# Optimization experiments

Hardware: AMD Instinct MI355X
Metric: run time of the kernel (lower is better)

## Reference

```python
import jax, jax.numpy as jnp
import numpy as np

THRESHOLD = 0.5
NEG_POS_RATIO = 3


def cxcy_to_xy(c):
    return jnp.concatenate([c[..., :2] - c[..., 2:] / 2.0, c[..., :2] + c[..., 2:] / 2.0], axis=-1)


def xy_to_cxcy(b):
    return jnp.concatenate([(b[..., :2] + b[..., 2:]) / 2.0, b[..., 2:] - b[..., :2]], axis=-1)


def cxcy_to_gcxgcy(c, p):
    # standard SSD encoding with variances (0.1, 0.2)
    return jnp.concatenate([
        (c[..., :2] - p[..., :2]) / (p[..., 2:] / 10.0),
        jnp.log(c[..., 2:] / p[..., 2:]) * 5.0,
    ], axis=-1)


def jaccard(a, b):
    # a: [n,4] xy boxes, b: [m,4] xy boxes -> [n,m] IoU
    lo = jnp.maximum(a[:, None, :2], b[None, :, :2])
    hi = jnp.minimum(a[:, None, 2:], b[None, :, 2:])
    wh = jnp.clip(hi - lo, 0.0)
    inter = wh[..., 0] * wh[..., 1]
    area_a = (a[:, 2] - a[:, 0]) * (a[:, 3] - a[:, 1])
    area_b = (b[:, 2] - b[:, 0]) * (b[:, 3] - b[:, 1])
    return inter / (area_a[:, None] + area_b[None, :] - inter)


def match_one(boxes_i, labels_i, priors_xy, priors_cxcy):
    # boxes_i: [O,4], labels_i: [O] -> true_locs [P,4], true_classes [P]
    n_obj = boxes_i.shape[0]
    ov = jaccard(boxes_i, priors_xy)                 # [O, P]
    ov_per_prior = ov.max(axis=0)                    # [P]
    obj_idx = jnp.argmax(ov, axis=0)                 # [P]
    prior_per_obj = jnp.argmax(ov, axis=1)           # [O]
    # force each object to own its best prior (scatter overwrite)
    obj_idx = obj_idx.at[prior_per_obj].set(jnp.arange(n_obj))
    ov_per_prior = ov_per_prior.at[prior_per_obj].set(1.0)
    lab = labels_i[obj_idx]                          # [P]
    lab = jnp.where(ov_per_prior < THRESHOLD, 0, lab)
    true_locs = cxcy_to_gcxgcy(xy_to_cxcy(boxes_i[obj_idx]), priors_cxcy)
    return true_locs, lab


def setup_inputs() -> dict:
    key = jax.random.key(0)
    ks = jax.random.split(key, 7)
    B, P, C, O = 64, 8732, 81, 32
    predicted_locs = jax.random.normal(ks[0], (B, P, 4), jnp.float32)
    predicted_scores = jax.random.normal(ks[1], (B, P, C), jnp.float32)
    ctr = jax.random.uniform(ks[2], (B, O, 2), jnp.float32, 0.2, 0.8)
    wh = jax.random.uniform(ks[3], (B, O, 2), jnp.float32, 0.05, 0.3)
    boxes = jnp.concatenate([ctr - wh / 2.0, ctr + wh / 2.0], axis=-1)  # valid xy boxes
    labels = jax.random.randint(ks[4], (B, O), 1, C)                    # nonzero object classes
    pctr = jax.random.uniform(ks[5], (P, 2), jnp.float32, 0.05, 0.95)
    pwh = jax.random.uniform(ks[6], (P, 2), jnp.float32, 0.05, 0.5)
    priors_cxcy = jnp.concatenate([pctr, pwh], axis=-1)
    return {
        'predicted_locs': predicted_locs,
        'predicted_scores': predicted_scores,
        'boxes': boxes,
        'labels': labels,
        'priors_cxcy': priors_cxcy,
    }


def reference(predicted_locs, predicted_scores, boxes, labels, priors_cxcy):
    priors_xy = cxcy_to_xy(priors_cxcy)
    true_locs, true_classes = jax.vmap(match_one, in_axes=(0, 0, None, None))(
        boxes, labels, priors_xy, priors_cxcy)       # [B,P,4], [B,P]

    log_probs = jax.nn.log_softmax(predicted_scores, axis=2)   # [B,P,C]
    bg_loss = -log_probs[:, :, 0]                               # mining score (detached in torch)

    pos_mask = true_classes > 0                                 # [B,P]
    num_pos = pos_mask.sum(axis=1, keepdims=True)               # [B,1]
    num_neg = NEG_POS_RATIO * num_pos
    mined = jnp.where(pos_mask, -jnp.inf, bg_loss)
    idx = jnp.argsort(-mined, axis=1)
    order = jnp.argsort(idx, axis=1)                            # rank of each prior by hardness
    neg_mask = order < num_neg
    mask = pos_mask | neg_mask

    # cross-entropy (sum over selected priors)
    ce = -jnp.take_along_axis(log_probs, true_classes[..., None], axis=2)[..., 0]  # [B,P]
    classification_loss = jnp.sum(ce * mask)

    # smooth-L1 (beta=1, sum over positive priors)
    diff = jnp.abs(predicted_locs - true_locs)
    sl1 = jnp.where(diff < 1.0, 0.5 * diff * diff, diff - 0.5)  # [B,P,4]
    smooth_l1_loss = jnp.sum(sl1.sum(axis=-1) * pos_mask)

    n = num_pos.sum().astype(predicted_locs.dtype)
    return classification_loss / n, smooth_l1_loss / n
```

## Files before the change

kernel.cpp:

```cpp
#include <hip/hip_runtime.h>
#include <stdint.h>

#define NB 64
#define NP 8732
#define NO 32
#define NC 81
#define NTOT (NB*NP)
#define THRESH 0.5f

typedef unsigned long long ull;

__global__ void k_init(float* cls_acc, float* sl1_acc, int* n_acc) {
    if (threadIdx.x == 0) { *cls_acc = 0.f; *sl1_acc = 0.f; *n_acc = 0; }
}

__global__ __launch_bounds__(512)
void k_match(const float4* __restrict__ boxes4, const int* __restrict__ labels,
             const float4* __restrict__ priors4, const float4* __restrict__ plocs4,
             int* __restrict__ lab_ws, int* __restrict__ numpos_ws,
             float* __restrict__ sl1_acc, int* __restrict__ n_acc)
{
#pragma clang fp contract(off)
    const int b   = blockIdx.x;
    const int tid = threadIdx.x;
    const int lane = tid & 63, wv = tid >> 6;

    __shared__ float         ov_s[NP];
    __shared__ unsigned char oi_s[NP];
    __shared__ float bx[NO][4];
    __shared__ float barea[NO];
    __shared__ int   blab[NO];
    __shared__ int   ppo[NO];
    __shared__ ull   red[8][8];
    __shared__ float redf[8];
    __shared__ int   redi[8];

    if (tid < NO) {
        float4 bb = boxes4[b*NO + tid];
        bx[tid][0] = bb.x; bx[tid][1] = bb.y; bx[tid][2] = bb.z; bx[tid][3] = bb.w;
        barea[tid] = (bb.z - bb.x) * (bb.w - bb.y);
        blab[tid]  = labels[b*NO + tid];
    }
    __syncthreads();

    for (int c = 0; c < 4; ++c) {
        ull bkey[8];
#pragma unroll
        for (int o8 = 0; o8 < 8; ++o8) bkey[o8] = 0ull;

        for (int p = tid; p < NP; p += 512) {
            float4 pr = priors4[p];
            float px1 = pr.x - pr.z*0.5f, py1 = pr.y - pr.w*0.5f;
            float px2 = pr.x + pr.z*0.5f, py2 = pr.y + pr.w*0.5f;
            float parea = (px2-px1)*(py2-py1);
            float bestv; int besto;
            if (c == 0) { bestv = -1.0f; besto = 0; }
            else        { bestv = ov_s[p]; besto = oi_s[p]; }
#pragma unroll
            for (int o8 = 0; o8 < 8; ++o8) {
                const int o = c*8 + o8;
                float lx = fmaxf(bx[o][0], px1), ly = fmaxf(bx[o][1], py1);
                float hx = fminf(bx[o][2], px2), hy = fminf(bx[o][3], py2);
                float w = fmaxf(hx - lx, 0.0f), h = fmaxf(hy - ly, 0.0f);
                float inter = w*h;
                float iou = inter / ((barea[o] + parea) - inter);
                if (iou > bestv) { bestv = iou; besto = o; }
                ull key = ((ull)__float_as_uint(iou) << 32) | (unsigned int)(~p);
                if (key > bkey[o8]) bkey[o8] = key;
            }
            ov_s[p] = bestv;
            oi_s[p] = (unsigned char)besto;
        }
#pragma unroll
        for (int o8 = 0; o8 < 8; ++o8) {
            ull k = bkey[o8];
            for (int off = 32; off > 0; off >>= 1) {
                ull other = __shfl_down(k, (unsigned)off);
                if (other > k) k = other;
            }
            if (lane == 0) red[o8][wv] = k;
        }
        __syncthreads();
        if (tid < 8) {
            ull k = red[tid][0];
#pragma unroll
            for (int w = 1; w < 8; ++w) if (red[tid][w] > k) k = red[tid][w];
            ppo[c*8 + tid] = (int)(~(unsigned int)(k & 0xFFFFFFFFull));
        }
        __syncthreads();
    }

    if (tid == 0) {
        for (int o = 0; o < NO; ++o) {
            int p = ppo[o];
            oi_s[p] = (unsigned char)o;
            ov_s[p] = 1.0f;
        }
    }
    __syncthreads();

    int cnt = 0; float sl1 = 0.0f;
    for (int p = tid; p < NP; p += 512) {
        float ov = ov_s[p];
        int   oi = oi_s[p];
        int   lb = (ov < THRESH) ? 0 : blab[oi];
        lab_ws[b*NP + p] = lb;
        if (lb > 0) {
            cnt++;
            float x1 = bx[oi][0], y1 = bx[oi][1], x2 = bx[oi][2], y2 = bx[oi][3];
            float bcx = (x1+x2)*0.5f, bcy = (y1+y2)*0.5f;
            float bw = x2-x1, bh = y2-y1;
            float4 pr = priors4[p];
            float g0 = (bcx - pr.x) / (pr.z / 10.0f);
            float g1 = (bcy - pr.y) / (pr.w / 10.0f);
            float g2 = logf(bw / pr.z) * 5.0f;
            float g3 = logf(bh / pr.w) * 5.0f;
            float4 pl = plocs4[(size_t)b*NP + p];
            float d0 = fabsf(pl.x-g0), d1 = fabsf(pl.y-g1);
            float d2 = fabsf(pl.z-g2), d3 = fabsf(pl.w-g3);
            sl1 += (d0 < 1.f ? 0.5f*d0*d0 : d0-0.5f);
            sl1 += (d1 < 1.f ? 0.5f*d1*d1 : d1-0.5f);
            sl1 += (d2 < 1.f ? 0.5f*d2*d2 : d2-0.5f);
            sl1 += (d3 < 1.f ? 0.5f*d3*d3 : d3-0.5f);
        }
    }
    for (int off = 32; off > 0; off >>= 1) {
        cnt += __shfl_down(cnt, (unsigned)off);
        sl1 += __shfl_down(sl1, (unsigned)off);
    }
    if (lane == 0) { redi[wv] = cnt; redf[wv] = sl1; }
    __syncthreads();
    if (tid == 0) {
        int c = 0; float s = 0.f;
#pragma unroll
        for (int w = 0; w < 8; ++w) { c += redi[w]; s += redf[w]; }
        numpos_ws[b] = c;
        atomicAdd(n_acc, c);
        atomicAdd(sl1_acc, s);
    }
}

#define CLS_BLOCKS 2048
__global__ __launch_bounds__(256)
void k_cls(const float* __restrict__ scores, const int* __restrict__ lab_ws,
           unsigned int* __restrict__ mined, float* __restrict__ cls_acc)
{
    const int lane = threadIdx.x & 63, wv = threadIdx.x >> 6;
    const int wave_gid = blockIdx.x*4 + wv;
    const int nw = CLS_BLOCKS*4;
    float ce_acc = 0.f;

    for (int r = wave_gid; r < NTOT; r += nw) {
        const float* s = scores + (size_t)r*NC;
        float v0 = s[lane];
        float v1 = (lane < NC-64) ? s[64+lane] : -INFINITY;
        float m = fmaxf(v0, v1);
#pragma unroll
        for (int off = 32; off > 0; off >>= 1) m = fmaxf(m, __shfl_xor(m, off));
        float e = expf(v0 - m) + ((lane < NC-64) ? expf(v1 - m) : 0.f);
#pragma unroll
        for (int off = 32; off > 0; off >>= 1) e += __shfl_xor(e, off);
        float lse = m + logf(e);

        int lb = lab_ws[r];
        unsigned int key = 0u;
        if (lb > 0) {
            float sv = (lb < 64) ? __shfl(v0, lb) : __shfl(v1, lb - 64);
            if (lane == 0) ce_acc += lse - sv;
        } else {
            key = __float_as_uint(lse - __shfl(v0, 0));
        }
        if (lane == 0) mined[r] = key;
    }

    __shared__ float redf[4];
    if (lane == 0) redf[wv] = ce_acc;
    __syncthreads();
    if (threadIdx.x == 0) atomicAdd(cls_acc, redf[0]+redf[1]+redf[2]+redf[3]);
}

__global__ __launch_bounds__(256)
void k_mine(const unsigned int* __restrict__ mined, const int* __restrict__ numpos_ws,
            float* __restrict__ cls_acc)
{
    const int b = blockIdx.x, tid = threadIdx.x;
    __shared__ unsigned int keys[NP];
    __shared__ unsigned int hist[256];
    __shared__ unsigned int suf[256];
    __shared__ unsigned int sh_prefix, sh_cnt;
    __shared__ float redf[4];

    for (int i = tid; i < NP; i += 256) keys[i] = mined[b*NP + i];
    const int np = numpos_ws[b];
    int k = 3*np;
    const int nneg = NP - np;
    if (k > nneg) k = nneg;
    __syncthreads();
    if (k <= 0) return;

    unsigned int prefix = 0, cnthi = 0;
    for (int pass = 0; pass < 4; ++pass) {
        const int shift = 24 - 8*pass;
        hist[tid] = 0;
        __syncthreads();
        for (int i = tid; i < NP; i += 256) {
            unsigned int u = keys[i];
            unsigned int hb = (pass == 0) ? 0u : (u >> (shift + 8));
            if (hb == prefix) atomicAdd(&hist[(u >> shift) & 255u], 1u);
        }
        __syncthreads();
        suf[tid] = hist[tid];
        __syncthreads();
#pragma unroll
        for (int off = 1; off < 256; off <<= 1) {
            unsigned int v = suf[tid] + ((tid + off < 256) ? suf[tid + off] : 0u);
            __syncthreads();
            suf[tid] = v;
            __syncthreads();
        }
        {
            unsigned int S = suf[tid];
            unsigned int c = cnthi + (S - hist[tid]);
            if (c < (unsigned)k && c + hist[tid] >= (unsigned)k) {
                sh_prefix = (prefix << 8) | (unsigned)tid;
                sh_cnt = c;
            }
        }
        __syncthreads();
        prefix = sh_prefix; cnthi = sh_cnt;
        __syncthreads();
    }

    const unsigned int uk = prefix;
    float sum = 0.f;
    for (int i = tid; i < NP; i += 256) {
        unsigned int u = keys[i];
        if (u > uk) sum += __uint_as_float(u);
    }
    for (int off = 32; off > 0; off >>= 1) sum += __shfl_down(sum, (unsigned)off);
    const int lane = tid & 63, wv = tid >> 6;
    if (lane == 0) redf[wv] = sum;
    __syncthreads();
    if (tid == 0) {
        float tot = redf[0]+redf[1]+redf[2]+redf[3];
        tot += (float)(k - (int)cnthi) * __uint_as_float(uk);
        atomicAdd(cls_acc, tot);
    }
}

__global__ void k_final(const float* cls_acc, const float* sl1_acc,
                        const int* n_acc, float* out)
{
    if (threadIdx.x == 0) {
        float n = (float)(*n_acc);
        out[0] = *cls_acc / n;
        out[1] = *sl1_acc / n;
    }
}

extern "C" void kernel_launch(void* const* d_in, const int* in_sizes, int n_in,
                              void* d_out, int out_size, void* d_ws, size_t ws_size,
                              hipStream_t stream)
{
    const float4* plocs4  = (const float4*)d_in[0];
    const float*  scores  = (const float*) d_in[1];
    const float4* boxes4  = (const float4*)d_in[2];
    const int*    labels  = (const int*)   d_in[3];
    const float4* priors4 = (const float4*)d_in[4];
    float* out = (float*)d_out;

    int*          lab_ws  = (int*)d_ws;
    unsigned int* mined   = (unsigned int*)d_ws + NTOT;
    int*          numpos  = (int*)((unsigned int*)d_ws + 2*NTOT);
    float*        cls_acc = (float*)(numpos + NB);
    float*        sl1_acc = cls_acc + 1;
    int*          n_acc   = (int*)(sl1_acc + 1);

    k_init <<<1, 64, 0, stream>>>(cls_acc, sl1_acc, n_acc);
    k_match<<<NB, 512, 0, stream>>>(boxes4, labels, priors4, plocs4,
                                    lab_ws, numpos, sl1_acc, n_acc);
    k_cls  <<<CLS_BLOCKS, 256, 0, stream>>>(scores, lab_ws, mined, cls_acc);
    k_mine <<<NB, 256, 0, stream>>>(mined, numpos, cls_acc);
    k_final<<<1, 64, 0, stream>>>(cls_acc, sl1_acc, n_acc, out);
}
```

Measured before the change: 432.6 us.

## Split matching across segments, pack rows per wave in softmax, bitwise top-k select

Matching is split into two kernels: eight segment blocks per image compute IoU against all 32 objects in one pass, storing a packed byte per prior and a per-segment best-prior key, and a second kernel merges the keys and computes smooth-L1. The classification kernel handles four prior rows per wave with 16 lanes each, uses fast exp/log intrinsics, and reads compact byte labels instead of int labels. Hard-negative selection switches from a 4-pass radix histogram to a 31-step bitwise threshold search. Global atomics and the init kernel are replaced by per-block partial sums reduced in the final kernel, which fixes summation order. The fast intrinsics may shift rounding slightly.

```diff
diff --git a/kernel.cpp b/kernel.cpp
--- a/kernel.cpp
+++ b/kernel.cpp
@@ -7,106 +7,129 @@
 #define NC 81
 #define NTOT (NB*NP)
 #define THRESH 0.5f
+#define NSEG 8
+#define SEGP 1092
+#define CLS_BLOCKS 2048
+#define NGRP (NTOT/4)
 
 typedef unsigned long long ull;
-
-__global__ void k_init(float* cls_acc, float* sl1_acc, int* n_acc) {
-    if (threadIdx.x == 0) { *cls_acc = 0.f; *sl1_acc = 0.f; *n_acc = 0; }
-}
-
-__global__ __launch_bounds__(512)
-void k_match(const float4* __restrict__ boxes4, const int* __restrict__ labels,
-             const float4* __restrict__ priors4, const float4* __restrict__ plocs4,
-             int* __restrict__ lab_ws, int* __restrict__ numpos_ws,
-             float* __restrict__ sl1_acc, int* __restrict__ n_acc)
+typedef unsigned int uint;
+
+__global__ __launch_bounds__(256)
+void k_match1(const float4* __restrict__ boxes4, const float4* __restrict__ priors4,
+              unsigned char* __restrict__ pp_g, ull* __restrict__ bkey_part)
 {
 #pragma clang fp contract(off)
-    const int b   = blockIdx.x;
-    const int tid = threadIdx.x;
+    const int b    = blockIdx.x >> 3;
+    const int seg  = blockIdx.x & 7;
+    const int tid  = threadIdx.x;
     const int lane = tid & 63, wv = tid >> 6;
-
-    __shared__ float         ov_s[NP];
-    __shared__ unsigned char oi_s[NP];
+    const int p0 = seg * SEGP;
+    const int p1 = (p0 + SEGP < NP) ? (p0 + SEGP) : NP;
+
     __shared__ float bx[NO][4];
     __shared__ float barea[NO];
-    __shared__ int   blab[NO];
-    __shared__ int   ppo[NO];
-    __shared__ ull   red[8][8];
-    __shared__ float redf[8];
-    __shared__ int   redi[8];
+    __shared__ ull   red[NO][4];
 
     if (tid < NO) {
         float4 bb = boxes4[b*NO + tid];
-        bx[tid][0] = bb.x; bx[tid][1] = bb.y; bx[tid][2] = bb.z; bx[tid][3] = bb.w;
-        barea[tid] = (bb.z - bb.x) * (bb.w - bb.y);
-        blab[tid]  = labels[b*NO + tid];
-    }
-    __syncthreads();
-
-    for (int c = 0; c < 4; ++c) {
-        ull bkey[8];
-#pragma unroll
-        for (int o8 = 0; o8 < 8; ++o8) bkey[o8] = 0ull;
-
-        for (int p = tid; p < NP; p += 512) {
-            float4 pr = priors4[p];
-            float px1 = pr.x - pr.z*0.5f, py1 = pr.y - pr.w*0.5f;
-            float px2 = pr.x + pr.z*0.5f, py2 = pr.y + pr.w*0.5f;
-            float parea = (px2-px1)*(py2-py1);
-            float bestv; int besto;
-            if (c == 0) { bestv = -1.0f; besto = 0; }
-            else        { bestv = ov_s[p]; besto = oi_s[p]; }
-#pragma unroll
-            for (int o8 = 0; o8 < 8; ++o8) {
-                const int o = c*8 + o8;
-                float lx = fmaxf(bx[o][0], px1), ly = fmaxf(bx[o][1], py1);
-                float hx = fminf(bx[o][2], px2), hy = fminf(bx[o][3], py2);
-                float w = fmaxf(hx - lx, 0.0f), h = fmaxf(hy - ly, 0.0f);
-                float inter = w*h;
-                float iou = inter / ((barea[o] + parea) - inter);
-                if (iou > bestv) { bestv = iou; besto = o; }
-                ull key = ((ull)__float_as_uint(iou) << 32) | (unsigned int)(~p);
-                if (key > bkey[o8]) bkey[o8] = key;
-            }
-            ov_s[p] = bestv;
-            oi_s[p] = (unsigned char)besto;
-        }
-#pragma unroll
-        for (int o8 = 0; o8 < 8; ++o8) {
-            ull k = bkey[o8];
-            for (int off = 32; off > 0; off >>= 1) {
-                ull other = __shfl_down(k, (unsigned)off);
-                if (other > k) k = other;
-            }
-            if (lane == 0) red[o8][wv] = k;
-        }
-        __syncthreads();
-        if (tid < 8) {
-            ull k = red[tid][0];
-#pragma unroll
-            for (int w = 1; w < 8; ++w) if (red[tid][w] > k) k = red[tid][w];
-            ppo[c*8 + tid] = (int)(~(unsigned int)(k & 0xFFFFFFFFull));
-        }
-        __syncthreads();
-    }
-
-    if (tid == 0) {
+        bx[tid][0]=bb.x; bx[tid][1]=bb.y; bx[tid][2]=bb.z; bx[tid][3]=bb.w;
+        barea[tid] = (bb.z-bb.x)*(bb.w-bb.y);
+    }
+    __syncthreads();
+
+    ull bkey[NO];
+#pragma unroll
+    for (int o = 0; o < NO; ++o) bkey[o] = 0ull;
+
+    for (int p = p0 + tid; p < p1; p += 256) {
+        float4 pr = priors4[p];
+        float px1 = pr.x - pr.z*0.5f, py1 = pr.y - pr.w*0.5f;
+        float px2 = pr.x + pr.z*0.5f, py2 = pr.y + pr.w*0.5f;
+        float parea = (px2-px1)*(py2-py1);
+        float bestv = -1.0f; int besto = 0;
+#pragma unroll
         for (int o = 0; o < NO; ++o) {
-            int p = ppo[o];
-            oi_s[p] = (unsigned char)o;
-            ov_s[p] = 1.0f;
+            float lx = fmaxf(bx[o][0], px1), ly = fmaxf(bx[o][1], py1);
+            float hx = fminf(bx[o][2], px2), hy = fminf(bx[o][3], py2);
+            float w = fmaxf(hx - lx, 0.0f), h = fmaxf(hy - ly, 0.0f);
+            float inter = w*h;
+            float iou = inter / ((barea[o] + parea) - inter);
+            if (iou > bestv) { bestv = iou; besto = o; }
+            ull key = ((ull)__float_as_uint(iou) << 32) | (uint)(~p);
+            if (key > bkey[o]) bkey[o] = key;
+        }
+        pp_g[(size_t)b*NP + p] =
+            (unsigned char)(besto | ((bestv < THRESH) ? 0 : 0x80));
+    }
+
+#pragma unroll
+    for (int o = 0; o < NO; ++o) {
+        ull k = bkey[o];
+        for (int off = 32; off > 0; off >>= 1) {
+            ull t = __shfl_down(k, (unsigned)off);
+            if (t > k) k = t;
+        }
+        if (lane == 0) red[o][wv] = k;
+    }
+    __syncthreads();
+    if (tid < NO) {
+        ull k = red[tid][0];
+#pragma unroll
+        for (int w = 1; w < 4; ++w) if (red[tid][w] > k) k = red[tid][w];
+        bkey_part[(b*NO + tid)*NSEG + seg] = k;
+    }
+}
+
+__global__ __launch_bounds__(256)
+void k_match2(const float4* __restrict__ boxes4, const int* __restrict__ labels,
+              const float4* __restrict__ priors4, const float4* __restrict__ plocs4,
+              const ull* __restrict__ bkey_part, unsigned char* __restrict__ pp_g,
+              int* __restrict__ numpos, float* __restrict__ sl1_part)
+{
+#pragma clang fp contract(off)
+    const int b = blockIdx.x, tid = threadIdx.x;
+    const int lane = tid & 63, wv = tid >> 6;
+
+    __shared__ uint  pp_u[NP/4];
+    __shared__ float bx[NO][4];
+    __shared__ int   ppo[NO];
+    __shared__ float redf[4];
+    __shared__ int   redi[4];
+    unsigned char* pp_s = (unsigned char*)pp_u;
+
+    const uint* src = (const uint*)(pp_g + (size_t)b*NP);
+    for (int i = tid; i < NP/4; i += 256) pp_u[i] = src[i];
+
+    if (tid < NO) {
+        float4 bb = boxes4[b*NO + tid];
+        bx[tid][0]=bb.x; bx[tid][1]=bb.y; bx[tid][2]=bb.z; bx[tid][3]=bb.w;
+        const ull* bp = bkey_part + (b*NO + tid)*NSEG;
+        ull k = bp[0];
+#pragma unroll
+        for (int s = 1; s < NSEG; ++s) if (bp[s] > k) k = bp[s];
+        ppo[tid] = (int)(~(uint)(k & 0xFFFFFFFFull));
+    }
+    __syncthreads();
+
+    if (tid < NO) {
+        int p = ppo[tid];
+        bool win = true;
+        for (int o2 = tid + 1; o2 < NO; ++o2) if (ppo[o2] == p) { win = false; break; }
+        if (win) {
+            unsigned char v = (unsigned char)(tid | 0x80);
+            pp_s[p] = v;
+            pp_g[(size_t)b*NP + p] = v;
         }
     }
     __syncthreads();
 
     int cnt = 0; float sl1 = 0.0f;
-    for (int p = tid; p < NP; p += 512) {
-        float ov = ov_s[p];
-        int   oi = oi_s[p];
-        int   lb = (ov < THRESH) ? 0 : blab[oi];
-        lab_ws[b*NP + p] = lb;
-        if (lb > 0) {
+    for (int p = tid; p < NP; p += 256) {
+        int ppv = pp_s[p];
+        if (ppv & 0x80) {
             cnt++;
+            int oi = ppv & 31;
             float x1 = bx[oi][0], y1 = bx[oi][1], x2 = bx[oi][2], y2 = bx[oi][3];
             float bcx = (x1+x2)*0.5f, bcy = (y1+y2)*0.5f;
             float bw = x2-x1, bh = y2-y1;
@@ -131,130 +154,133 @@
     if (lane == 0) { redi[wv] = cnt; redf[wv] = sl1; }
     __syncthreads();
     if (tid == 0) {
-        int c = 0; float s = 0.f;
-#pragma unroll
-        for (int w = 0; w < 8; ++w) { c += redi[w]; s += redf[w]; }
-        numpos_ws[b] = c;
-        atomicAdd(n_acc, c);
-        atomicAdd(sl1_acc, s);
-    }
-}
-
-#define CLS_BLOCKS 2048
-__global__ __launch_bounds__(256)
-void k_cls(const float* __restrict__ scores, const int* __restrict__ lab_ws,
-           unsigned int* __restrict__ mined, float* __restrict__ cls_acc)
-{
-    const int lane = threadIdx.x & 63, wv = threadIdx.x >> 6;
-    const int wave_gid = blockIdx.x*4 + wv;
-    const int nw = CLS_BLOCKS*4;
+        numpos[b]   = redi[0]+redi[1]+redi[2]+redi[3];
+        sl1_part[b] = redf[0]+redf[1]+redf[2]+redf[3];
+    }
+}
+
+__global__ __launch_bounds__(256)
+void k_cls(const float* __restrict__ scores, const unsigned char* __restrict__ pp_g,
+           const int* __restrict__ labels, uint* __restrict__ mined,
+           float* __restrict__ ce_part)
+{
+    const int tid = threadIdx.x, lane = tid & 63, wv = tid >> 6;
+    const int sub = lane >> 4, sl = lane & 15;
+    const int wgid = blockIdx.x*4 + wv;
     float ce_acc = 0.f;
 
-    for (int r = wave_gid; r < NTOT; r += nw) {
+    for (int grp = wgid; grp < NGRP; grp += CLS_BLOCKS*4) {
+        const int r = grp*4 + sub;
         const float* s = scores + (size_t)r*NC;
-        float v0 = s[lane];
-        float v1 = (lane < NC-64) ? s[64+lane] : -INFINITY;
-        float m = fmaxf(v0, v1);
-#pragma unroll
-        for (int off = 32; off > 0; off >>= 1) m = fmaxf(m, __shfl_xor(m, off));
-        float e = expf(v0 - m) + ((lane < NC-64) ? expf(v1 - m) : 0.f);
-#pragma unroll
-        for (int off = 32; off > 0; off >>= 1) e += __shfl_xor(e, off);
-        float lse = m + logf(e);
-
-        int lb = lab_ws[r];
-        unsigned int key = 0u;
-        if (lb > 0) {
-            float sv = (lb < 64) ? __shfl(v0, lb) : __shfl(v1, lb - 64);
-            if (lane == 0) ce_acc += lse - sv;
-        } else {
-            key = __float_as_uint(lse - __shfl(v0, 0));
-        }
-        if (lane == 0) mined[r] = key;
-    }
-
+        float v0 = s[sl], v1 = s[16+sl], v2 = s[32+sl], v3 = s[48+sl], v4 = s[64+sl];
+        float v5 = (sl == 0) ? s[80] : -INFINITY;
+        float m = fmaxf(fmaxf(fmaxf(v0,v1), fmaxf(v2,v3)), fmaxf(v4,v5));
+#pragma unroll
+        for (int off = 8; off > 0; off >>= 1) m = fmaxf(m, __shfl_xor(m, off));
+        float e = __expf(v0-m)+__expf(v1-m)+__expf(v2-m)+__expf(v3-m)+__expf(v4-m);
+        if (sl == 0) e += __expf(v5-m);
+#pragma unroll
+        for (int off = 8; off > 0; off >>= 1) e += __shfl_xor(e, off);
+        float lse = m + __logf(e);
+
+        if (sl == 0) {
+            int ppv = pp_g[r];
+            uint key = 0u;
+            if (ppv & 0x80) {
+                int bb = r / NP;
+                int lb = labels[bb*NO + (ppv & 31)];
+                float sv = scores[(size_t)r*NC + lb];
+                ce_acc += lse - sv;
+            } else {
+                key = __float_as_uint(lse - v0);
+            }
+            mined[r] = key;
+        }
+    }
+
+    for (int off = 32; off > 0; off >>= 1) ce_acc += __shfl_down(ce_acc, (unsigned)off);
     __shared__ float redf[4];
     if (lane == 0) redf[wv] = ce_acc;
     __syncthreads();
-    if (threadIdx.x == 0) atomicAdd(cls_acc, redf[0]+redf[1]+redf[2]+redf[3]);
-}
-
-__global__ __launch_bounds__(256)
-void k_mine(const unsigned int* __restrict__ mined, const int* __restrict__ numpos_ws,
-            float* __restrict__ cls_acc)
+    if (tid == 0) ce_part[blockIdx.x] = redf[0]+redf[1]+redf[2]+redf[3];
+}
+
+__global__ __launch_bounds__(256)
+void k_mine(const uint* __restrict__ mined, const int* __restrict__ numpos,
+            float* __restrict__ mined_sum)
 {
     const int b = blockIdx.x, tid = threadIdx.x;
-    __shared__ unsigned int keys[NP];
-    __shared__ unsigned int hist[256];
-    __shared__ unsigned int suf[256];
-    __shared__ unsigned int sh_prefix, sh_cnt;
+    const int lane = tid & 63, wv = tid >> 6;
+    __shared__ uint keys[NP];
+    __shared__ int  redi[4];
     __shared__ float redf[4];
 
-    for (int i = tid; i < NP; i += 256) keys[i] = mined[b*NP + i];
-    const int np = numpos_ws[b];
+    {
+        const uint4* src = (const uint4*)(mined + (size_t)b*NP);
+        uint4* dst = (uint4*)keys;
+        for (int i = tid; i < NP/4; i += 256) dst[i] = src[i];
+    }
+    const int np = numpos[b];
     int k = 3*np;
     const int nneg = NP - np;
     if (k > nneg) k = nneg;
     __syncthreads();
-    if (k <= 0) return;
-
-    unsigned int prefix = 0, cnthi = 0;
-    for (int pass = 0; pass < 4; ++pass) {
-        const int shift = 24 - 8*pass;
-        hist[tid] = 0;
+    if (k <= 0) { if (tid == 0) mined_sum[b] = 0.f; return; }
+
+    uint uk = 0u;
+    for (int bit = 30; bit >= 0; --bit) {
+        uint cand = uk | (1u << bit);
+        int c = 0;
+        for (int i = tid; i < NP; i += 256) c += (keys[i] >= cand) ? 1 : 0;
+        for (int off = 32; off > 0; off >>= 1) c += __shfl_down(c, (unsigned)off);
+        if (lane == 0) redi[wv] = c;
         __syncthreads();
-        for (int i = tid; i < NP; i += 256) {
-            unsigned int u = keys[i];
-            unsigned int hb = (pass == 0) ? 0u : (u >> (shift + 8));
-            if (hb == prefix) atomicAdd(&hist[(u >> shift) & 255u], 1u);
-        }
+        int tot = redi[0]+redi[1]+redi[2]+redi[3];
+        if (tot >= k) uk = cand;
         __syncthreads();
-        suf[tid] = hist[tid];
-        __syncthreads();
-#pragma unroll
-        for (int off = 1; off < 256; off <<= 1) {
-            unsigned int v = suf[tid] + ((tid + off < 256) ? suf[tid + off] : 0u);
-            __syncthreads();
-            suf[tid] = v;
-            __syncthreads();
-        }
-        {
-            unsigned int S = suf[tid];
-            unsigned int c = cnthi + (S - hist[tid]);
-            if (c < (unsigned)k && c + hist[tid] >= (unsigned)k) {
-                sh_prefix = (prefix << 8) | (unsigned)tid;
-                sh_cnt = c;
-            }
-        }
-        __syncthreads();
-        prefix = sh_prefix; cnthi = sh_cnt;
-        __syncthreads();
-    }
-
-    const unsigned int uk = prefix;
-    float sum = 0.f;
+    }
+
+    int cgt = 0; float sum = 0.f;
     for (int i = tid; i < NP; i += 256) {
-        unsigned int u = keys[i];
-        if (u > uk) sum += __uint_as_float(u);
-    }
-    for (int off = 32; off > 0; off >>= 1) sum += __shfl_down(sum, (unsigned)off);
-    const int lane = tid & 63, wv = tid >> 6;
-    if (lane == 0) redf[wv] = sum;
+        uint u = keys[i];
+        if (u > uk) { cgt++; sum += __uint_as_float(u); }
+    }
+    for (int off = 32; off > 0; off >>= 1) {
+        cgt += __shfl_down(cgt, (unsigned)off);
+        sum += __shfl_down(sum, (unsigned)off);
+    }
+    if (lane == 0) { redi[wv] = cgt; redf[wv] = sum; }
     __syncthreads();
     if (tid == 0) {
-        float tot = redf[0]+redf[1]+redf[2]+redf[3];
-        tot += (float)(k - (int)cnthi) * __uint_as_float(uk);
-        atomicAdd(cls_acc, tot);
-    }
-}
-
-__global__ void k_final(const float* cls_acc, const float* sl1_acc,
-                        const int* n_acc, float* out)
-{
-    if (threadIdx.x == 0) {
-        float n = (float)(*n_acc);
-        out[0] = *cls_acc / n;
-        out[1] = *sl1_acc / n;
+        int   c = redi[0]+redi[1]+redi[2]+redi[3];
+        float s = redf[0]+redf[1]+redf[2]+redf[3];
+        mined_sum[b] = s + (float)(k - c) * __uint_as_float(uk);
+    }
+}
+
+__global__ __launch_bounds__(256)
+void k_final(const float* __restrict__ ce_part, const float* __restrict__ mined_sum,
+             const float* __restrict__ sl1_part, const int* __restrict__ numpos,
+             float* __restrict__ out)
+{
+    const int tid = threadIdx.x, lane = tid & 63, wv = tid >> 6;
+    float c = 0.f, s = 0.f; int n = 0;
+    for (int i = tid; i < CLS_BLOCKS; i += 256) c += ce_part[i];
+    if (tid < NB) { c += mined_sum[tid]; s = sl1_part[tid]; n = numpos[tid]; }
+    for (int off = 32; off > 0; off >>= 1) {
+        c += __shfl_down(c, (unsigned)off);
+        s += __shfl_down(s, (unsigned)off);
+        n += __shfl_down(n, (unsigned)off);
+    }
+    __shared__ float rc[4], rs[4]; __shared__ int rn[4];
+    if (lane == 0) { rc[wv] = c; rs[wv] = s; rn[wv] = n; }
+    __syncthreads();
+    if (tid == 0) {
+        float cc = rc[0]+rc[1]+rc[2]+rc[3];
+        float ss = rs[0]+rs[1]+rs[2]+rs[3];
+        float nn = (float)(rn[0]+rn[1]+rn[2]+rn[3]);
+        out[0] = cc / nn;
+        out[1] = ss / nn;
     }
 }
 
@@ -269,17 +295,19 @@
     const float4* priors4 = (const float4*)d_in[4];
     float* out = (float*)d_out;
 
-    int*          lab_ws  = (int*)d_ws;
-    unsigned int* mined   = (unsigned int*)d_ws + NTOT;
-    int*          numpos  = (int*)((unsigned int*)d_ws + 2*NTOT);
-    float*        cls_acc = (float*)(numpos + NB);
-    float*        sl1_acc = cls_acc + 1;
-    int*          n_acc   = (int*)(sl1_acc + 1);
-
-    k_init <<<1, 64, 0, stream>>>(cls_acc, sl1_acc, n_acc);
-    k_match<<<NB, 512, 0, stream>>>(boxes4, labels, priors4, plocs4,
-                                    lab_ws, numpos, sl1_acc, n_acc);
-    k_cls  <<<CLS_BLOCKS, 256, 0, stream>>>(scores, lab_ws, mined, cls_acc);
-    k_mine <<<NB, 256, 0, stream>>>(mined, numpos, cls_acc);
-    k_final<<<1, 64, 0, stream>>>(cls_acc, sl1_acc, n_acc, out);
-}
+    uint* w = (uint*)d_ws;
+    unsigned char* pp_g   = (unsigned char*)w;
+    uint*          mined  = w + NTOT/4;
+    ull*           bkeyp  = (ull*)(w + NTOT/4 + NTOT);
+    int*           numpos = (int*)(bkeyp + NB*NO*NSEG);
+    float*         sl1p   = (float*)(numpos + NB);
+    float*         msum   = sl1p + NB;
+    float*         cep    = msum + NB;
+
+    k_match1<<<NB*NSEG,    256, 0, stream>>>(boxes4, priors4, pp_g, bkeyp);
+    k_match2<<<NB,         256, 0, stream>>>(boxes4, labels, priors4, plocs4,
+                                             bkeyp, pp_g, numpos, sl1p);
+    k_cls   <<<CLS_BLOCKS, 256, 0, stream>>>(scores, pp_g, labels, mined, cep);
+    k_mine  <<<NB,         256, 0, stream>>>(mined, numpos, msum);
+    k_final <<<1,          256, 0, stream>>>(cep, msum, sl1p, numpos, out);
+}
```

Measured after the change: 370.0 us. 1.17x faster.
